# Kernel tuning notes

Measured on AMD Instinct MI355X. Metric: run time of the kernel, lower is better.

Reference implementation:

```python
import jax, jax.numpy as jnp
import numpy as np

L, E, H, R = 6, 1024, 8, 33
DH = E // H
FF = 4 * E
B, S = 8, 512


def _layer_norm(x, g, b, eps=1e-5):
    m = jnp.mean(x, axis=-1, keepdims=True)
    v = jnp.mean(jnp.square(x - m), axis=-1, keepdims=True)
    return (x - m) * jax.lax.rsqrt(v + eps) * g + b


def setup_inputs() -> dict:
    key = jax.random.key(0)
    ks = jax.random.split(key, 24)
    rn = lambda k, shape, s=0.02: (jax.random.normal(k, shape, jnp.float32) * s)
    inp = {
        'enc_padded': jax.random.normal(ks[0], (B, S, E), jnp.float32),
        'relations': jax.random.randint(ks[1], (B, S, S), 0, R),
        'enc_lengths': jax.random.randint(ks[2], (B,), 1, S + 1),
        'Wq': rn(ks[3], (L, E, E)), 'bq': jnp.zeros((L, E), jnp.float32),
        'Wk': rn(ks[4], (L, E, E)), 'bk': jnp.zeros((L, E), jnp.float32),
        'Wv': rn(ks[5], (L, E, E)), 'bv': jnp.zeros((L, E), jnp.float32),
        'Wo': rn(ks[6], (L, E, E)), 'bo': jnp.zeros((L, E), jnp.float32),
        'rel_k': rn(ks[7], (L, R, DH)),
        'rel_v': rn(ks[8], (L, R, DH)),
        'W1': rn(ks[9], (L, E, FF)), 'b1': jnp.zeros((L, FF), jnp.float32),
        'W2': rn(ks[10], (L, FF, E)), 'b2': jnp.zeros((L, E), jnp.float32),
        'ln1_g': jnp.ones((L, E), jnp.float32), 'ln1_b': jnp.zeros((L, E), jnp.float32),
        'ln2_g': jnp.ones((L, E), jnp.float32), 'ln2_b': jnp.zeros((L, E), jnp.float32),
        'lnf_g': jnp.ones((E,), jnp.float32), 'lnf_b': jnp.zeros((E,), jnp.float32),
    }
    return inp


def reference(enc_padded, relations, enc_lengths, Wq, bq, Wk, bk, Wv, bv, Wo, bo,
              rel_k, rel_v, W1, b1, W2, b2, ln1_g, ln1_b, ln2_g, ln2_b, lnf_g, lnf_b):
    x = enc_padded  # [B,S,E]
    dt = x.dtype
    # attention mask: valid iff both query and key positions are within seq length
    pos = jnp.arange(S)
    valid = pos[None, :] < enc_lengths[:, None]            # [B,S]
    mask2d = valid[:, :, None] & valid[:, None, :]          # [B,S,S]
    # one-hot relation indicator, shared across layers (R=33 is small)
    rel_oh = jax.nn.one_hot(relations, R, dtype=dt)        # [B,S,S,R]
    scale = 1.0 / np.sqrt(DH).astype(np.float32)

    def split_heads(t):  # [B,S,E] -> [B,H,S,DH]
        return t.reshape(B, S, H, DH).transpose(0, 2, 1, 3)

    for l in range(L):
        # --- relation-aware self-attention (pre-LN sublayer) ---
        h = _layer_norm(x, ln1_g[l], ln1_b[l])
        q = split_heads(h @ Wq[l] + bq[l])
        k = split_heads(h @ Wk[l] + bk[l])
        v = split_heads(h @ Wv[l] + bv[l])
        scores = jnp.einsum('bhid,bhjd->bhij', q, k)
        # relation key bias: q_i . rel_k[rel[i,j]]  via small [B,H,S,R] GEMM + one-hot contraction
        qr = jnp.einsum('bhid,rd->bhir', q, rel_k[l])
        scores = (scores + jnp.einsum('bhir,bijr->bhij', qr, rel_oh)) * scale
        scores = jnp.where(mask2d[:, None], scores, jnp.asarray(-1e9, dt))
        attn = jax.nn.softmax(scores, axis=-1)              # [B,H,S,S]
        out = jnp.einsum('bhij,bhjd->bhid', attn, v)
        # relation value bias: sum_j attn_ij * rel_v[rel[i,j]]
        a_rel = jnp.einsum('bhij,bijr->bhir', attn, rel_oh)
        out = out + jnp.einsum('bhir,rd->bhid', a_rel, rel_v[l])
        out = out.transpose(0, 2, 1, 3).reshape(B, S, E) @ Wo[l] + bo[l]
        x = x + out
        # --- position-wise feed-forward (pre-LN sublayer) ---
        h2 = _layer_norm(x, ln2_g[l], ln2_b[l])
        x = x + (jax.nn.relu(h2 @ W1[l] + b1[l]) @ W2[l] + b2[l])
    return _layer_norm(x, lnf_g, lnf_b)
```

## Files before the change

kernel.cpp:

```cpp
#include <hip/hip_runtime.h>

#define LNUM 6
#define EDIM 1024
#define HNUM 8
#define DHD  128
#define RNUM 33
#define FFD  4096
#define BNUM 8
#define SLEN 512
#define TOK  (BNUM*SLEN)

typedef __attribute__((ext_vector_type(8))) short bf16x8;
typedef __attribute__((ext_vector_type(4))) float f32x4;
typedef unsigned short u16;
typedef unsigned int u32;

__device__ __forceinline__ u16 f2b(float f) {
  u32 u = __builtin_bit_cast(u32, f);
  u32 r = u + 0x7FFFu + ((u >> 16) & 1u);
  return (u16)(r >> 16);
}
__device__ __forceinline__ u32 pck(float a, float b) { return (u32)f2b(a) | ((u32)f2b(b) << 16); }

#define GL16(gp, lp) __builtin_amdgcn_global_load_lds(                        \
    (const __attribute__((address_space(1))) void*)(gp),                      \
    (__attribute__((address_space(3))) void*)(lp), 16, 0, 0)

#define WAITVM8 do { asm volatile("s_waitcnt vmcnt(8)" ::: "memory"); \
                     __builtin_amdgcn_sched_barrier(0); } while (0)
#define WAITVM4 do { asm volatile("s_waitcnt vmcnt(4)" ::: "memory"); \
                     __builtin_amdgcn_sched_barrier(0); } while (0)
#define WAITVM0 do { asm volatile("s_waitcnt vmcnt(0)" ::: "memory"); \
                     __builtin_amdgcn_sched_barrier(0); } while (0)

template<int BF16OUT>
__global__ __launch_bounds__(256) void ln_kernel(const float* __restrict__ x,
                                                 const float* __restrict__ g,
                                                 const float* __restrict__ be,
                                                 void* __restrict__ o) {
  int row = blockIdx.x;
  int t = threadIdx.x;
  const float* xr = x + (size_t)row * EDIM;
  float4 xv = *reinterpret_cast<const float4*>(xr + t * 4);
  float s1 = xv.x + xv.y + xv.z + xv.w;
  float s2 = xv.x*xv.x + xv.y*xv.y + xv.z*xv.z + xv.w*xv.w;
#pragma unroll
  for (int off = 32; off >= 1; off >>= 1) {
    s1 += __shfl_down(s1, off, 64);
    s2 += __shfl_down(s2, off, 64);
  }
  __shared__ float r1[4], r2[4];
  if ((t & 63) == 0) { r1[t >> 6] = s1; r2[t >> 6] = s2; }
  __syncthreads();
  s1 = r1[0] + r1[1] + r1[2] + r1[3];
  s2 = r2[0] + r2[1] + r2[2] + r2[3];
  float mean = s1 * (1.0f / EDIM);
  float var  = s2 * (1.0f / EDIM) - mean * mean;
  float rstd = rsqrtf(var + 1e-5f);
  float4 gv = *reinterpret_cast<const float4*>(g + t * 4);
  float4 bv = *reinterpret_cast<const float4*>(be + t * 4);
  float o0 = (xv.x - mean) * rstd * gv.x + bv.x;
  float o1 = (xv.y - mean) * rstd * gv.y + bv.y;
  float o2 = (xv.z - mean) * rstd * gv.z + bv.z;
  float o3 = (xv.w - mean) * rstd * gv.w + bv.w;
  if (BF16OUT) {
    ushort4 ov; ov.x = f2b(o0); ov.y = f2b(o1); ov.z = f2b(o2); ov.w = f2b(o3);
    *reinterpret_cast<ushort4*>((u16*)o + (size_t)row * EDIM + t * 4) = ov;
  } else {
    *reinterpret_cast<float4*>((float*)o + (size_t)row * EDIM + t * 4) = make_float4(o0, o1, o2, o3);
  }
}

__global__ __launch_bounds__(256) void wtrans(const float* __restrict__ src0,
                                              u16* __restrict__ dst0,
                                              int Kd, int Nd, size_t sstride, size_t dstride) {
  __shared__ float Ts[32][33];
  const float* src = src0 + blockIdx.z * sstride;
  u16* dst = dst0 + blockIdx.z * dstride;
  int r0 = blockIdx.y * 32, c0 = blockIdx.x * 32;
  int ty = threadIdx.x >> 3, tx = threadIdx.x & 7;
  float4 v = *reinterpret_cast<const float4*>(src + (size_t)(r0 + ty) * Nd + c0 + tx * 4);
  Ts[ty][tx*4+0] = v.x; Ts[ty][tx*4+1] = v.y; Ts[ty][tx*4+2] = v.z; Ts[ty][tx*4+3] = v.w;
  __syncthreads();
  ushort4 o;
  o.x = f2b(Ts[tx*4+0][ty]); o.y = f2b(Ts[tx*4+1][ty]);
  o.z = f2b(Ts[tx*4+2][ty]); o.w = f2b(Ts[tx*4+3][ty]);
  *reinterpret_cast<ushort4*>(dst + (size_t)(c0 + ty) * Kd + r0 + tx * 4) = o;
}

__global__ __launch_bounds__(256) void relpack(const int* __restrict__ rel,
                                               unsigned char* __restrict__ out) {
  __shared__ int Ts[32][33];
  int bz = blockIdx.z;
  int r0 = blockIdx.y * 32, c0 = blockIdx.x * 32;
  int ty = threadIdx.x >> 3, tx = threadIdx.x & 7;
  const int* src = rel + (size_t)bz * SLEN * SLEN;
  int4 v = *reinterpret_cast<const int4*>(src + (size_t)(r0 + ty) * SLEN + c0 + tx * 4);
  Ts[ty][tx*4+0] = v.x; Ts[ty][tx*4+1] = v.y; Ts[ty][tx*4+2] = v.z; Ts[ty][tx*4+3] = v.w;
  __syncthreads();
  u32 o = (u32)(Ts[tx*4+0][ty] & 255) | ((u32)(Ts[tx*4+1][ty] & 255) << 8) |
          ((u32)(Ts[tx*4+2][ty] & 255) << 16) | ((u32)(Ts[tx*4+3][ty] & 255) << 24);
  *reinterpret_cast<u32*>(out + (size_t)bz * SLEN * SLEN + (size_t)(c0 + ty) * SLEN + r0 + tx * 4) = o;
}

template<int DEPTH, int BIASMODE, int ACT, int RES, int OUTBF16>
__global__ __launch_bounds__(512, 4) void gemm_bt(const u16* __restrict__ A,
                                                  const u16* __restrict__ B,
                                                  const float* __restrict__ bias0,
                                                  const float* __restrict__ bias1,
                                                  const float* __restrict__ res,
                                                  void* __restrict__ Cv,
                                                  int M, int N, int K) {
  __shared__ u16 As[DEPTH][128 * 64];
  __shared__ u16 Bs[DEPTH][128 * 64];
  int t = threadIdx.x;
  int l = t & 63, w = t >> 6;
  int wm = w >> 2, wn = w & 3;
  int m0 = blockIdx.y * 128, n0 = blockIdx.x * 128;
  f32x4 acc[4][2] = {};
  const u16* Agp = A + (size_t)(m0 + w * 16 + (l >> 3)) * K + (l & 7) * 8;
  const u16* Bgp = B + (size_t)(n0 + w * 16 + (l >> 3)) * K + (l & 7) * 8;
  const int nst = K >> 6;
  auto issue = [&](int k0, int bi) {
#pragma unroll
    for (int u = 0; u < 2; ++u) {
      GL16(Agp + (size_t)(u * 8) * K + k0, &As[bi][w * 1024 + u * 512]);
      GL16(Bgp + (size_t)(u * 8) * K + k0, &Bs[bi][w * 1024 + u * 512]);
    }
  };
  issue(0, 0);
  if (DEPTH == 3 && nst > 1) issue(64, 1);
  for (int i = 0; i < nst; ++i) {
    int cur = (DEPTH == 3) ? (i % 3) : (i & 1);
    if (DEPTH == 3) {
      if (i + 2 < nst)      { issue((i + 2) * 64, (i + 2) % 3); WAITVM8; }
      else if (i + 1 < nst) { WAITVM4; }
      else                  { WAITVM0; }
    } else {
      if (i + 1 < nst) { issue((i + 1) * 64, cur ^ 1); WAITVM4; }
      else             { WAITVM0; }
    }
    __builtin_amdgcn_s_barrier();
    const u16* Asc = As[cur];
    const u16* Bsc = Bs[cur];
#pragma unroll
    for (int d4 = 0; d4 < 2; ++d4) {
      bf16x8 af[4];
#pragma unroll
      for (int fm = 0; fm < 4; ++fm) {
        int row = wm * 64 + fm * 16 + (l & 15);
        af[fm] = *reinterpret_cast<const bf16x8*>(Asc + row * 64 + (d4 * 4 + (l >> 4)) * 8);
      }
#pragma unroll
      for (int fn = 0; fn < 2; ++fn) {
        int row = wn * 32 + fn * 16 + (l & 15);
        bf16x8 bf = *reinterpret_cast<const bf16x8*>(Bsc + row * 64 + (d4 * 4 + (l >> 4)) * 8);
#pragma unroll
        for (int fm = 0; fm < 4; ++fm)
          acc[fm][fn] = __builtin_amdgcn_mfma_f32_16x16x32_bf16(af[fm], bf, acc[fm][fn], 0, 0, 0);
      }
    }
    __builtin_amdgcn_s_barrier();
  }
#pragma unroll
  for (int fm = 0; fm < 4; ++fm)
#pragma unroll
    for (int fn = 0; fn < 2; ++fn)
#pragma unroll
      for (int e = 0; e < 4; ++e) {
        int m = m0 + wm * 64 + fm * 16 + (l >> 4) * 4 + e;
        int n = n0 + wn * 32 + fn * 16 + (l & 15);
        float v = acc[fm][fn][e];
        if (BIASMODE == 0) v += bias0[n];
        if (BIASMODE == 1) v += bias0[m];
        if (BIASMODE == 2) v += (n < 1024) ? bias0[n] : bias1[n - 1024];
        if (ACT == 1) v = fmaxf(v, 0.f);
        if (RES == 1) v += res[(size_t)m * N + n];
        if (OUTBF16) ((u16*)Cv)[(size_t)m * N + n] = f2b(v);
        else ((float*)Cv)[(size_t)m * N + n] = v;
      }
}

template<int BIASMODE, int ACT, int RES, int OUTBF16>
__global__ __launch_bounds__(512, 2) void gemm_big(const u16* __restrict__ A,
                                                   const u16* __restrict__ B,
                                                   const float* __restrict__ bias0,
                                                   const float* __restrict__ res,
                                                   void* __restrict__ Cv,
                                                   int M, int N, int K) {
  __shared__ u16 As[2][256 * 64];
  __shared__ u16 Bs[2][256 * 64];
  int t = threadIdx.x;
  int l = t & 63, w = t >> 6;
  int wm = w >> 2, wn = w & 3;
  int m0 = blockIdx.y * 256, n0 = blockIdx.x * 256;
  f32x4 acc[8][4] = {};
  const u16* Agp = A + (size_t)(m0 + w * 32 + (l >> 3)) * K + (l & 7) * 8;
  const u16* Bgp = B + (size_t)(n0 + w * 32 + (l >> 3)) * K + (l & 7) * 8;
  const int nst = K >> 6;
  auto issue = [&](int k0, int bi) {
#pragma unroll
    for (int u = 0; u < 4; ++u) {
      GL16(Agp + (size_t)(u * 8) * K + k0, &As[bi][w * 2048 + u * 512]);
      GL16(Bgp + (size_t)(u * 8) * K + k0, &Bs[bi][w * 2048 + u * 512]);
    }
  };
  issue(0, 0);
  for (int i = 0; i < nst; ++i) {
    int cur = i & 1;
    if (i + 1 < nst) { issue((i + 1) * 64, cur ^ 1); WAITVM8; }
    else             { WAITVM0; }
    __builtin_amdgcn_s_barrier();
    const u16* Asc = As[cur];
    const u16* Bsc = Bs[cur];
#pragma unroll
    for (int d4 = 0; d4 < 2; ++d4) {
      bf16x8 bf[4];
#pragma unroll
      for (int fn = 0; fn < 4; ++fn) {
        int row = wn * 64 + fn * 16 + (l & 15);
        bf[fn] = *reinterpret_cast<const bf16x8*>(Bsc + row * 64 + (d4 * 4 + (l >> 4)) * 8);
      }
#pragma unroll
      for (int fm = 0; fm < 8; ++fm) {
        int row = wm * 128 + fm * 16 + (l & 15);
        bf16x8 af = *reinterpret_cast<const bf16x8*>(Asc + row * 64 + (d4 * 4 + (l >> 4)) * 8);
#pragma unroll
        for (int fn = 0; fn < 4; ++fn)
          acc[fm][fn] = __builtin_amdgcn_mfma_f32_16x16x32_bf16(af, bf[fn], acc[fm][fn], 0, 0, 0);
      }
    }
    __builtin_amdgcn_s_barrier();
  }
#pragma unroll
  for (int fm = 0; fm < 8; ++fm)
#pragma unroll
    for (int fn = 0; fn < 4; ++fn)
#pragma unroll
      for (int e = 0; e < 4; ++e) {
        int m = m0 + wm * 128 + fm * 16 + (l >> 4) * 4 + e;
        int n = n0 + wn * 64 + fn * 16 + (l & 15);
        float v = acc[fm][fn][e];
        if (BIASMODE == 0) v += bias0[n];
        if (ACT == 1) v = fmaxf(v, 0.f);
        if (RES == 1) v += res[(size_t)m * N + n];
        if (OUTBF16) ((u16*)Cv)[(size_t)m * N + n] = f2b(v);
        else ((float*)Cv)[(size_t)m * N + n] = v;
      }
}

#define A_P  0
#define A_Q  16384
#define A_PS 32768
#define A_QR 43008
#define A_AR 52224
#define A_LS 61440
#define A_SM 61696

__global__ __launch_bounds__(256, 2) void attn_kernel(const u16* __restrict__ qk,
                                                      const u16* __restrict__ vt,
                                                      const unsigned char* __restrict__ rel8,
                                                      const int* __restrict__ lens,
                                                      const float* __restrict__ relk,
                                                      const float* __restrict__ relv,
                                                      u16* __restrict__ outb) {
  __align__(16) __shared__ char sm[A_SM];
  char*  Pb  = sm + A_P;
  char*  Qb  = sm + A_Q;
  char*  PSb = sm + A_PS;
  float* QR  = (float*)(sm + A_QR);
  float* AREL = (float*)(sm + A_AR);
  float* LSUM = (float*)(sm + A_LS);

  const int t = threadIdx.x;
  const int l = t & 63, w = t >> 6;
  const int lg = l >> 4;
  const int ll = l & 15;
  const int bx = blockIdx.x;
  const int xcd = bx & 7, rem = bx >> 3, slot = rem & 7, it = rem >> 3;
  const int g = slot * 8 + xcd;
  const int b = g >> 3, hh = g & 7;
  const int i0 = it * 64;
  const int len = lens[b];
  const float scale = 0.08838834764831845f;
  char* PSw = PSb + w * 2560;

  auto issueK = [&](int kt) {
#pragma unroll
    for (int u = 0; u < 4; ++u) {
      int row = w * 16 + u * 4 + (lg);
      int sb = (ll * 16) ^ (((u * 4 + lg) & 7) << 4);
      const u16* gp = qk + (size_t)(b * SLEN + kt * 64 + row) * 2048 + 1024 + hh * DHD + (sb >> 1);
      GL16(gp, Pb + (w * 4 + u) * 1024);
    }
  };
  auto issueV = [&](int kt) {
#pragma unroll
    for (int u = 0; u < 4; ++u) {
      int row = w * 32 + u * 8 + (l >> 3);
      int sb = ((l & 7) * 16) ^ ((l >> 3) << 4);
      const u16* gp = vt + (size_t)(hh * DHD + row) * TOK + b * SLEN + kt * 64 + (sb >> 1);
      GL16(gp, Qb + (w * 4 + u) * 1024);
    }
  };

  u32 relw[4];
  const unsigned char* relbase = rel8 + (size_t)b * SLEN * SLEN + (i0 + w * 16 + lg * 4);
  {
    const unsigned char* rb = relbase + (size_t)ll * SLEN;
#pragma unroll
    for (int fj = 0; fj < 4; ++fj)
      relw[fj] = *reinterpret_cast<const u32*>(rb + (size_t)(fj * 16) * SLEN);
  }
  for (int idx = l; idx < 16 * 36; idx += 64) AREL[w * 16 * 36 + idx] = 0.f;
  if (t < 192) {
    int r = t >> 2, sub = t & 3;
#pragma unroll
    for (int u = 0; u < 4; ++u) {
      int seg = sub * 4 + u;
      uint4 o;
      if (r < RNUM) {
        float4 f0 = *reinterpret_cast<const float4*>(relk + r * DHD + seg * 8);
        float4 f1 = *reinterpret_cast<const float4*>(relk + r * DHD + seg * 8 + 4);
        o.x = pck(f0.x, f0.y); o.y = pck(f0.z, f0.w);
        o.z = pck(f1.x, f1.y); o.w = pck(f1.z, f1.w);
      } else { o.x = o.y = o.z = o.w = 0u; }
      *reinterpret_cast<uint4*>(Pb + r * 256 + ((seg * 16) ^ ((r & 7) << 4))) = o;
    }
  }
  bf16x8 aq[4];
  {
    const u16* qrow = qk + (size_t)(b * SLEN + i0 + w * 16 + ll) * 2048 + hh * DHD;
#pragma unroll
    for (int d4 = 0; d4 < 4; ++d4)
      aq[d4] = *reinterpret_cast<const bf16x8*>(qrow + (d4 * 4 + lg) * 8);
  }
  __syncthreads();
#pragma unroll
  for (int rb = 0; rb < 3; ++rb) {
    f32x4 acc = {};
#pragma unroll
    for (int d4 = 0; d4 < 4; ++d4) {
      int rr = rb * 16 + ll;
      bf16x8 br = *reinterpret_cast<const bf16x8*>(Pb + rr * 256 + (((d4 * 4 + lg) * 16) ^ ((rr & 7) << 4)));
      acc = __builtin_amdgcn_mfma_f32_16x16x32_bf16(aq[d4], br, acc, 0, 0, 0);
    }
    int col = rb * 16 + ll;
    if (col < 36)
#pragma unroll
      for (int e = 0; e < 4; ++e)
        QR[(w * 16 + lg * 4 + e) * 36 + col] = acc[e];
  }
  __syncthreads();
  issueK(0);

  bool rowv[4];
#pragma unroll
  for (int e = 0; e < 4; ++e) rowv[e] = (i0 + w * 16 + lg * 4 + e) < len;

  float m_[4];
#pragma unroll
  for (int e = 0; e < 4; ++e) m_[e] = -3.0e38f;
  f32x4 oacc[8] = {};

  for (int kt = 0; kt < 8; ++kt) {
    issueV(kt);
    WAITVM4;
    __builtin_amdgcn_s_barrier();
    __builtin_amdgcn_s_setprio(1);
    f32x4 sacc[4];
#pragma unroll
    for (int fj = 0; fj < 4; ++fj) {
      f32x4 a = {};
#pragma unroll
      for (int d4 = 0; d4 < 4; ++d4) {
        int row = fj * 16 + ll;
        bf16x8 bk_ = *reinterpret_cast<const bf16x8*>(Pb + row * 256 + (((d4 * 4 + lg) * 16) ^ ((row & 7) << 4)));
        a = __builtin_amdgcn_mfma_f32_16x16x32_bf16(aq[d4], bk_, a, 0, 0, 0);
      }
      sacc[fj] = a;
    }
    __builtin_amdgcn_s_setprio(0);
#pragma unroll
    for (int fj = 0; fj < 4; ++fj) {
      bool colv = (kt * 64 + fj * 16 + ll) < len;
      u32 rw = relw[fj];
#pragma unroll
      for (int e = 0; e < 4; ++e) {
        int r = (rw >> (8 * e)) & 255;
        float s = (sacc[fj][e] + QR[(w * 16 + lg * 4 + e) * 36 + r]) * scale;
        s = (rowv[e] && colv) ? s : -1e9f;
        sacc[fj][e] = s;
      }
    }
    float pl[4];
#pragma unroll
    for (int e = 0; e < 4; ++e)
      pl[e] = fmaxf(fmaxf(sacc[0][e], sacc[1][e]), fmaxf(sacc[2][e], sacc[3][e]));
    bool ok = (pl[0] <= m_[0] + 8.f) && (pl[1] <= m_[1] + 8.f) &&
              (pl[2] <= m_[2] + 8.f) && (pl[3] <= m_[3] + 8.f);
    if (!__all(ok)) {
#pragma unroll
      for (int e = 0; e < 4; ++e) {
        float px = pl[e];
        px = fmaxf(px, __shfl_xor(px, 1, 64));
        px = fmaxf(px, __shfl_xor(px, 2, 64));
        px = fmaxf(px, __shfl_xor(px, 4, 64));
        px = fmaxf(px, __shfl_xor(px, 8, 64));
        float mn = fmaxf(m_[e], px);
        float f = __expf(m_[e] - mn);
        m_[e] = mn;
#pragma unroll
        for (int fd = 0; fd < 8; ++fd) oacc[fd][e] *= f;
        if (f != 1.0f) {
          int row = w * 16 + lg * 4 + e;
          AREL[row * 36 + ll] *= f;
          AREL[row * 36 + 16 + ll] *= f;
          if (ll == 0) AREL[row * 36 + 32] *= f;
        }
      }
    }
#pragma unroll
    for (int fj = 0; fj < 4; ++fj) {
      u32 rw = relw[fj];
#pragma unroll
      for (int e = 0; e < 4; ++e) {
        float p = __expf(sacc[fj][e] - m_[e]);
        int iloc = lg * 4 + e;
        atomicAdd(&AREL[(w * 16 + iloc) * 36 + ((rw >> (8 * e)) & 255)], p);
        *reinterpret_cast<u16*>(PSw + iloc * 136 + (fj * 16 + ll) * 2) = f2b(p);
      }
    }
    if (kt < 7) {
      const unsigned char* rb = relbase + (size_t)((kt + 1) * 64 + ll) * SLEN;
#pragma unroll
      for (int fj = 0; fj < 4; ++fj)
        relw[fj] = *reinterpret_cast<const u32*>(rb + (size_t)(fj * 16) * SLEN);
    }
    __builtin_amdgcn_s_barrier();
    if (kt < 7) issueK(kt + 1);
    if (kt < 7) { WAITVM8; } else { WAITVM0; }
    __builtin_amdgcn_s_barrier();
    __builtin_amdgcn_s_setprio(1);
#pragma unroll
    for (int kc = 0; kc < 2; ++kc) {
      bf16x8 pa = *reinterpret_cast<const bf16x8*>(PSw + ll * 136 + (kc * 4 + lg) * 16);
#pragma unroll
      for (int fd = 0; fd < 8; ++fd) {
        int row = fd * 16 + ll;
        bf16x8 vb = *reinterpret_cast<const bf16x8*>(Qb + row * 128 + (((kc * 4 + lg) * 16) ^ ((row & 7) << 4)));
        oacc[fd] = __builtin_amdgcn_mfma_f32_16x16x32_bf16(pa, vb, oacc[fd], 0, 0, 0);
      }
    }
    __builtin_amdgcn_s_setprio(0);
    __builtin_amdgcn_s_barrier();
  }
  if (l < 16) {
    int row = w * 16 + l;
    float s = 0.f;
    for (int r = 0; r < RNUM; ++r) s += AREL[row * 36 + r];
    LSUM[row] = s;
  }
#pragma unroll
  for (int e = 0; e < 4; ++e) {
    float inv = 1.0f / LSUM[w * 16 + lg * 4 + e];
#pragma unroll
    for (int fd = 0; fd < 8; ++fd) oacc[fd][e] *= inv;
  }
  for (int idx = t; idx < 128 * 64; idx += 256) {
    int d = idx >> 6, r = idx & 63;
    u16 v = (r < RNUM) ? f2b(relv[r * DHD + d]) : (u16)0;
    *reinterpret_cast<u16*>(Pb + d * 128 + ((r * 2) ^ ((d & 7) << 4))) = v;
  }
  for (int idx = l; idx < 1024; idx += 64) {
    int ri = idx >> 6, r = idx & 63;
    int row = w * 16 + ri;
    float v = (r < RNUM) ? AREL[row * 36 + r] * (1.0f / LSUM[row]) : 0.f;
    *reinterpret_cast<u16*>(PSw + ri * 128 + ((r * 2) ^ ((ri & 7) << 4))) = f2b(v);
  }
  __syncthreads();
#pragma unroll
  for (int kc = 0; kc < 2; ++kc) {
    bf16x8 pa = *reinterpret_cast<const bf16x8*>(PSw + ll * 128 + (((kc * 4 + lg) * 16) ^ ((ll & 7) << 4)));
#pragma unroll
    for (int fd = 0; fd < 8; ++fd) {
      int row = fd * 16 + ll;
      bf16x8 vb = *reinterpret_cast<const bf16x8*>(Pb + row * 128 + (((kc * 4 + lg) * 16) ^ ((row & 7) << 4)));
      oacc[fd] = __builtin_amdgcn_mfma_f32_16x16x32_bf16(pa, vb, oacc[fd], 0, 0, 0);
    }
  }
  char* OSw = Qb + w * 4096;
#pragma unroll
  for (int fd = 0; fd < 8; ++fd)
#pragma unroll
    for (int e = 0; e < 4; ++e)
      *reinterpret_cast<u16*>(OSw + ((lg * 4 + e) * 128 + fd * 16 + ll) * 2) = f2b(oacc[fd][e]);
  __syncthreads();
  {
    int ri = l >> 2, q4 = l & 3;
    const char* srcb = OSw + ri * 256 + q4 * 64;
    u16* dst = outb + (size_t)(b * SLEN + i0 + w * 16 + ri) * EDIM + hh * DHD + q4 * 32;
    uint4 x0 = *reinterpret_cast<const uint4*>(srcb);
    uint4 x1 = *reinterpret_cast<const uint4*>(srcb + 16);
    uint4 x2 = *reinterpret_cast<const uint4*>(srcb + 32);
    uint4 x3 = *reinterpret_cast<const uint4*>(srcb + 48);
    *reinterpret_cast<uint4*>(dst)      = x0;
    *reinterpret_cast<uint4*>(dst + 8)  = x1;
    *reinterpret_cast<uint4*>(dst + 16) = x2;
    *reinterpret_cast<uint4*>(dst + 24) = x3;
  }
}

extern "C" void kernel_launch(void* const* d_in, const int* in_sizes, int n_in,
                              void* d_out, int out_size, void* d_ws, size_t ws_size,
                              hipStream_t stream) {
  const float* enc  = (const float*)d_in[0];
  const int*   rel  = (const int*)d_in[1];
  const int*   lens = (const int*)d_in[2];
  const float* Wq = (const float*)d_in[3];
  const float* bq = (const float*)d_in[4];
  const float* Wk = (const float*)d_in[5];
  const float* bk = (const float*)d_in[6];
  const float* Wv = (const float*)d_in[7];
  const float* bv = (const float*)d_in[8];
  const float* Wo = (const float*)d_in[9];
  const float* bo = (const float*)d_in[10];
  const float* relk = (const float*)d_in[11];
  const float* relv = (const float*)d_in[12];
  const float* W1 = (const float*)d_in[13];
  const float* b1 = (const float*)d_in[14];
  const float* W2 = (const float*)d_in[15];
  const float* b2 = (const float*)d_in[16];
  const float* ln1g = (const float*)d_in[17];
  const float* ln1b = (const float*)d_in[18];
  const float* ln2g = (const float*)d_in[19];
  const float* ln2b = (const float*)d_in[20];
  const float* lnfg = (const float*)d_in[21];
  const float* lnfb = (const float*)d_in[22];
  float* out = (float*)d_out;

  char* W = (char*)d_ws;
  u16* h     = (u16*)W;
  unsigned char* rel8_h = (unsigned char*)W;
  char* U    = W + 8388608;
  u16* qkb   = (u16*)U;
  u16* vtb   = (u16*)(U + 16777216);
  u16* attno = (u16*)(U + 25165824);
  u16* mid   = (u16*)U;
  bool xin = ws_size >= (size_t)83886080;
  float* x = xin ? (float*)(W + 41943040) : out;
  size_t wt_off = xin ? 58720256 : 41943040;
  char* WT = W + wt_off;
  bool big = ws_size >= (size_t)209715200;

  const size_t EE = (size_t)EDIM * EDIM;
  const size_t EF = (size_t)EDIM * FFD;
  size_t wt_bytes = (big ? 6 : 1) * (size_t)(2*EE + EE + EE + EF + EF) * 2;
  bool rel_ded = ws_size >= wt_off + wt_bytes + (size_t)BNUM * SLEN * SLEN + 256;
  unsigned char* rel8 = rel_ded ? (unsigned char*)(WT + wt_bytes) : rel8_h;

  u16 *WqkT, *WvT, *WoT, *W1T, *W2T;
  dim3 blk(256);
  if (big) {
    u16* wqk_all = (u16*)WT;
    u16* wv_all  = wqk_all + 6 * 2 * EE;
    u16* wo_all  = wv_all + 6 * EE;
    u16* w1_all  = wo_all + 6 * EE;
    u16* w2_all  = w1_all + 6 * EF;
    wtrans<<<dim3(32, 32, 6), blk, 0, stream>>>(Wq, wqk_all, 1024, 1024, EE, 2 * EE);
    wtrans<<<dim3(32, 32, 6), blk, 0, stream>>>(Wk, wqk_all + EE, 1024, 1024, EE, 2 * EE);
    wtrans<<<dim3(32, 32, 6), blk, 0, stream>>>(Wv, wv_all, 1024, 1024, EE, EE);
    wtrans<<<dim3(32, 32, 6), blk, 0, stream>>>(Wo, wo_all, 1024, 1024, EE, EE);
    wtrans<<<dim3(128, 32, 6), blk, 0, stream>>>(W1, w1_all, 1024, 4096, EF, EF);
    wtrans<<<dim3(32, 128, 6), blk, 0, stream>>>(W2, w2_all, 4096, 1024, EF, EF);
    WqkT = wqk_all; WvT = wv_all; WoT = wo_all; W1T = w1_all; W2T = w2_all;
  } else {
    WqkT = (u16*)WT;
    WvT  = WqkT + 2 * EE;
    WoT  = WvT + EE;
    W1T  = WoT + EE;
    W2T  = W1T + EF;
  }
  if (rel_ded) relpack<<<dim3(16, 16, 8), blk, 0, stream>>>(rel, rel8);

  dim3 gLN(TOK);
  for (int ll = 0; ll < LNUM; ++ll) {
    u16 *wqkT, *wvT, *woT, *w1T, *w2T;
    if (big) {
      wqkT = WqkT + (size_t)ll * 2 * EE; wvT = WvT + (size_t)ll * EE; woT = WoT + (size_t)ll * EE;
      w1T = W1T + (size_t)ll * EF; w2T = W2T + (size_t)ll * EF;
    } else {
      wqkT = WqkT; wvT = WvT; woT = WoT; w1T = W1T; w2T = W2T;
      wtrans<<<dim3(32, 32, 1), blk, 0, stream>>>(Wq + ll * EE, wqkT, 1024, 1024, 0, 0);
      wtrans<<<dim3(32, 32, 1), blk, 0, stream>>>(Wk + ll * EE, wqkT + EE, 1024, 1024, 0, 0);
      wtrans<<<dim3(32, 32, 1), blk, 0, stream>>>(Wv + ll * EE, wvT, 1024, 1024, 0, 0);
      wtrans<<<dim3(32, 32, 1), blk, 0, stream>>>(Wo + ll * EE, woT, 1024, 1024, 0, 0);
      wtrans<<<dim3(128, 32, 1), blk, 0, stream>>>(W1 + ll * EF, w1T, 1024, 4096, 0, 0);
      wtrans<<<dim3(32, 128, 1), blk, 0, stream>>>(W2 + ll * EF, w2T, 4096, 1024, 0, 0);
    }
    const float* xin_p = (ll == 0) ? enc : x;
    ln_kernel<1><<<gLN, blk, 0, stream>>>(xin_p, ln1g + ll * EDIM, ln1b + ll * EDIM, h);
    gemm_bt<2, 2, 0, 0, 1><<<dim3(16, 32), dim3(512), 0, stream>>>(
        h, wqkT, bq + ll * EDIM, bk + ll * EDIM, nullptr, qkb, TOK, 2048, EDIM);
    gemm_bt<3, 1, 0, 0, 1><<<dim3(32, 8), dim3(512), 0, stream>>>(
        wvT, h, bv + ll * EDIM, nullptr, nullptr, vtb, EDIM, TOK, EDIM);
    if (!rel_ded) relpack<<<dim3(16, 16, 8), blk, 0, stream>>>(rel, rel8);
    attn_kernel<<<dim3(512), blk, 0, stream>>>(qkb, vtb, rel8, lens,
                                               relk + (size_t)ll * RNUM * DHD,
                                               relv + (size_t)ll * RNUM * DHD, attno);
    gemm_bt<3, 0, 0, 1, 0><<<dim3(8, 32), dim3(512), 0, stream>>>(
        attno, woT, bo + ll * EDIM, nullptr, xin_p, x, TOK, EDIM, EDIM);
    ln_kernel<1><<<gLN, blk, 0, stream>>>(x, ln2g + ll * EDIM, ln2b + ll * EDIM, h);
    gemm_big<0, 1, 0, 1><<<dim3(FFD / 256, TOK / 256), dim3(512), 0, stream>>>(
        h, w1T, b1 + ll * FFD, nullptr, mid, TOK, FFD, EDIM);
    gemm_bt<3, 0, 0, 1, 0><<<dim3(8, 32), dim3(512), 0, stream>>>(
        mid, w2T, b2 + ll * EDIM, nullptr, x, x, TOK, EDIM, FFD);
  }
  ln_kernel<0><<<gLN, blk, 0, stream>>>(x, lnfg, lnfb, out);
}
```

Baseline: 2.189 ms.

## XOR-swizzle GEMM LDS tiles, swizzle attention P buffer, reorder relation loads

Both GEMM kernels now store A and B tiles in LDS with an XOR swizzle applied at the global-to-LDS copy and undone at the fragment reads. The goal is to remove bank conflicts on the row-strided 16-byte reads. In the attention kernel, the per-wave probability buffer drops its padded 136-byte stride for a swizzled 128-byte stride, which also shrinks the LDS layout offsets. The relation-index loads move after the K/V async issues, with vmcnt waits adjusted to 20 so they overlap. That new wait count depends on the exact count of in-flight loads and could break correctness if it is wrong.

```diff
diff --git a/kernel.cpp b/kernel.cpp
--- a/kernel.cpp
+++ b/kernel.cpp
@@ -26,6 +26,8 @@
     (const __attribute__((address_space(1))) void*)(gp),                      \
     (__attribute__((address_space(3))) void*)(lp), 16, 0, 0)
 
+#define WAITVM20 do { asm volatile("s_waitcnt vmcnt(20)" ::: "memory"); \
+                      __builtin_amdgcn_sched_barrier(0); } while (0)
 #define WAITVM8 do { asm volatile("s_waitcnt vmcnt(8)" ::: "memory"); \
                      __builtin_amdgcn_sched_barrier(0); } while (0)
 #define WAITVM4 do { asm volatile("s_waitcnt vmcnt(4)" ::: "memory"); \
@@ -118,8 +120,9 @@
   int wm = w >> 2, wn = w & 3;
   int m0 = blockIdx.y * 128, n0 = blockIdx.x * 128;
   f32x4 acc[4][2] = {};
-  const u16* Agp = A + (size_t)(m0 + w * 16 + (l >> 3)) * K + (l & 7) * 8;
-  const u16* Bgp = B + (size_t)(n0 + w * 16 + (l >> 3)) * K + (l & 7) * 8;
+  const int sc = (((l & 7) ^ ((l >> 3) & 7))) * 8;
+  const u16* Agp = A + (size_t)(m0 + w * 16 + (l >> 3)) * K + sc;
+  const u16* Bgp = B + (size_t)(n0 + w * 16 + (l >> 3)) * K + sc;
   const int nst = K >> 6;
   auto issue = [&](int k0, int bi) {
 #pragma unroll
@@ -145,16 +148,17 @@
     const u16* Bsc = Bs[cur];
 #pragma unroll
     for (int d4 = 0; d4 < 2; ++d4) {
+      int c = d4 * 4 + (l >> 4);
       bf16x8 af[4];
 #pragma unroll
       for (int fm = 0; fm < 4; ++fm) {
         int row = wm * 64 + fm * 16 + (l & 15);
-        af[fm] = *reinterpret_cast<const bf16x8*>(Asc + row * 64 + (d4 * 4 + (l >> 4)) * 8);
+        af[fm] = *reinterpret_cast<const bf16x8*>(Asc + row * 64 + (c ^ (row & 7)) * 8);
       }
 #pragma unroll
       for (int fn = 0; fn < 2; ++fn) {
         int row = wn * 32 + fn * 16 + (l & 15);
-        bf16x8 bf = *reinterpret_cast<const bf16x8*>(Bsc + row * 64 + (d4 * 4 + (l >> 4)) * 8);
+        bf16x8 bf = *reinterpret_cast<const bf16x8*>(Bsc + row * 64 + (c ^ (row & 7)) * 8);
 #pragma unroll
         for (int fm = 0; fm < 4; ++fm)
           acc[fm][fn] = __builtin_amdgcn_mfma_f32_16x16x32_bf16(af[fm], bf, acc[fm][fn], 0, 0, 0);
@@ -195,8 +199,9 @@
   int wm = w >> 2, wn = w & 3;
   int m0 = blockIdx.y * 256, n0 = blockIdx.x * 256;
   f32x4 acc[8][4] = {};
-  const u16* Agp = A + (size_t)(m0 + w * 32 + (l >> 3)) * K + (l & 7) * 8;
-  const u16* Bgp = B + (size_t)(n0 + w * 32 + (l >> 3)) * K + (l & 7) * 8;
+  const int sc = (((l & 7) ^ ((l >> 3) & 7))) * 8;
+  const u16* Agp = A + (size_t)(m0 + w * 32 + (l >> 3)) * K + sc;
+  const u16* Bgp = B + (size_t)(n0 + w * 32 + (l >> 3)) * K + sc;
   const int nst = K >> 6;
   auto issue = [&](int k0, int bi) {
 #pragma unroll
@@ -215,16 +220,17 @@
     const u16* Bsc = Bs[cur];
 #pragma unroll
     for (int d4 = 0; d4 < 2; ++d4) {
+      int c = d4 * 4 + (l >> 4);
       bf16x8 bf[4];
 #pragma unroll
       for (int fn = 0; fn < 4; ++fn) {
         int row = wn * 64 + fn * 16 + (l & 15);
-        bf[fn] = *reinterpret_cast<const bf16x8*>(Bsc + row * 64 + (d4 * 4 + (l >> 4)) * 8);
+        bf[fn] = *reinterpret_cast<const bf16x8*>(Bsc + row * 64 + (c ^ (row & 7)) * 8);
       }
 #pragma unroll
       for (int fm = 0; fm < 8; ++fm) {
         int row = wm * 128 + fm * 16 + (l & 15);
-        bf16x8 af = *reinterpret_cast<const bf16x8*>(Asc + row * 64 + (d4 * 4 + (l >> 4)) * 8);
+        bf16x8 af = *reinterpret_cast<const bf16x8*>(Asc + row * 64 + (c ^ (row & 7)) * 8);
 #pragma unroll
         for (int fn = 0; fn < 4; ++fn)
           acc[fm][fn] = __builtin_amdgcn_mfma_f32_16x16x32_bf16(af, bf[fn], acc[fm][fn], 0, 0, 0);
@@ -252,10 +258,10 @@
 #define A_P  0
 #define A_Q  16384
 #define A_PS 32768
-#define A_QR 43008
-#define A_AR 52224
-#define A_LS 61440
-#define A_SM 61696
+#define A_QR 40960
+#define A_AR 50176
+#define A_LS 59392
+#define A_SM 59648
 
 __global__ __launch_bounds__(256, 2) void attn_kernel(const u16* __restrict__ qk,
                                                       const u16* __restrict__ vt,
@@ -283,7 +289,7 @@
   const int i0 = it * 64;
   const int len = lens[b];
   const float scale = 0.08838834764831845f;
-  char* PSw = PSb + w * 2560;
+  char* PSw = PSb + w * 2048;
 
   auto issueK = [&](int kt) {
 #pragma unroll
@@ -303,15 +309,8 @@
       GL16(gp, Qb + (w * 4 + u) * 1024);
     }
   };
-
-  u32 relw[4];
   const unsigned char* relbase = rel8 + (size_t)b * SLEN * SLEN + (i0 + w * 16 + lg * 4);
-  {
-    const unsigned char* rb = relbase + (size_t)ll * SLEN;
-#pragma unroll
-    for (int fj = 0; fj < 4; ++fj)
-      relw[fj] = *reinterpret_cast<const u32*>(rb + (size_t)(fj * 16) * SLEN);
-  }
+
   for (int idx = l; idx < 16 * 36; idx += 64) AREL[w * 16 * 36 + idx] = 0.f;
   if (t < 192) {
     int r = t >> 2, sub = t & 3;
@@ -353,6 +352,13 @@
   }
   __syncthreads();
   issueK(0);
+  u32 relw[4];
+  {
+    const unsigned char* rb = relbase + (size_t)ll * SLEN;
+#pragma unroll
+    for (int fj = 0; fj < 4; ++fj)
+      relw[fj] = *reinterpret_cast<const u32*>(rb + (size_t)(fj * 16) * SLEN);
+  }
 
   bool rowv[4];
 #pragma unroll
@@ -365,7 +371,7 @@
 
   for (int kt = 0; kt < 8; ++kt) {
     issueV(kt);
-    WAITVM4;
+    WAITVM20;
     __builtin_amdgcn_s_barrier();
     __builtin_amdgcn_s_setprio(1);
     f32x4 sacc[4];
@@ -428,23 +434,27 @@
         float p = __expf(sacc[fj][e] - m_[e]);
         int iloc = lg * 4 + e;
         atomicAdd(&AREL[(w * 16 + iloc) * 36 + ((rw >> (8 * e)) & 255)], p);
-        *reinterpret_cast<u16*>(PSw + iloc * 136 + (fj * 16 + ll) * 2) = f2b(p);
-      }
-    }
+        *reinterpret_cast<u16*>(PSw + iloc * 128 + (((fj * 16 + ll) * 2) ^ ((iloc & 7) << 4))) = f2b(p);
+      }
+    }
+    __builtin_amdgcn_s_barrier();
     if (kt < 7) {
-      const unsigned char* rb = relbase + (size_t)((kt + 1) * 64 + ll) * SLEN;
-#pragma unroll
-      for (int fj = 0; fj < 4; ++fj)
-        relw[fj] = *reinterpret_cast<const u32*>(rb + (size_t)(fj * 16) * SLEN);
-    }
-    __builtin_amdgcn_s_barrier();
-    if (kt < 7) issueK(kt + 1);
-    if (kt < 7) { WAITVM8; } else { WAITVM0; }
+      issueK(kt + 1);
+      {
+        const unsigned char* rb = relbase + (size_t)((kt + 1) * 64 + ll) * SLEN;
+#pragma unroll
+        for (int fj = 0; fj < 4; ++fj)
+          relw[fj] = *reinterpret_cast<const u32*>(rb + (size_t)(fj * 16) * SLEN);
+      }
+      WAITVM20;
+    } else {
+      WAITVM0;
+    }
     __builtin_amdgcn_s_barrier();
     __builtin_amdgcn_s_setprio(1);
 #pragma unroll
     for (int kc = 0; kc < 2; ++kc) {
-      bf16x8 pa = *reinterpret_cast<const bf16x8*>(PSw + ll * 136 + (kc * 4 + lg) * 16);
+      bf16x8 pa = *reinterpret_cast<const bf16x8*>(PSw + ll * 128 + (((kc * 4 + lg) * 16) ^ ((ll & 7) << 4)));
 #pragma unroll
       for (int fd = 0; fd < 8; ++fd) {
         int row = fd * 16 + ll;
```

Measured after the change: 1.936 ms, median of 2. 1.13x faster.
